# Performance work log

Measured on AMD Instinct MI355X. Metric: run time of the kernel, lower is better.

## Reference

```python
import jax, jax.numpy as jnp
import numpy as np

NUM_ENT = 40000
NUM_REL = 20


def _rgcn_layer(x, src, dst, et, comp, basis, root, bias, act):
    # Basis decomposition: W_r = sum_b comp[r, b] * basis[b]  -> [R, in, out]
    W = jnp.einsum('rb,bio->rio', comp, basis)
    # Per-(dst, relation) sum of source features: equivalent to per-edge
    # transform W_{et[e]} @ x[src[e]] then scatter-sum, but transforms after
    # aggregation (linear, so identical math) to avoid an [E, in, out] gather.
    seg = dst * NUM_REL + et                       # combined segment id
    S = jax.ops.segment_sum(x[src], seg, num_segments=NUM_ENT * NUM_REL)
    S = S.reshape(NUM_ENT, NUM_REL, x.shape[1])    # [N, R, in]
    agg = jnp.einsum('nri,rio->no', S, W)          # [N, out]
    # mean aggregation over ALL incoming edges (PyG RGCNConv aggr='mean')
    deg = jax.ops.segment_sum(jnp.ones(src.shape[0], x.dtype), dst,
                              num_segments=NUM_ENT)
    agg = agg / jnp.clip(deg, 1.0)[:, None]
    out = agg + x @ root + bias
    return jnp.tanh(out) if act else out


def setup_inputs() -> dict:
    key = jax.random.key(0)
    ks = jax.random.split(key, 16)
    E = 640000
    d = 128
    B = 8
    s = 0.05
    return {
        'edge_index': jax.random.randint(ks[0], (2, E), 0, NUM_ENT),
        'edge_type': jax.random.randint(ks[1], (E,), 0, NUM_REL),
        'init_embed': jax.random.normal(ks[2], (NUM_ENT, d), jnp.float32) * s,
        'init_rel': jax.random.normal(ks[3], (NUM_REL * 2, d), jnp.float32) * s,
        'w_rel': jax.random.normal(ks[4], (d, d), jnp.float32) * s,
        'comp1': jax.random.normal(ks[5], (NUM_REL, B), jnp.float32) * s,
        'basis1': jax.random.normal(ks[6], (B, d, d), jnp.float32) * s,
        'root1': jax.random.normal(ks[7], (d, d), jnp.float32) * s,
        'bias1': jax.random.normal(ks[8], (d,), jnp.float32) * s,
        'comp2': jax.random.normal(ks[9], (NUM_REL, B), jnp.float32) * s,
        'basis2': jax.random.normal(ks[10], (B, d, d), jnp.float32) * s,
        'root2': jax.random.normal(ks[11], (d, d), jnp.float32) * s,
        'bias2': jax.random.normal(ks[12], (d,), jnp.float32) * s,
    }


def reference(edge_index, edge_type, init_embed, init_rel, w_rel,
              comp1, basis1, root1, bias1, comp2, basis2, root2, bias2):
    src, dst = edge_index[0], edge_index[1]
    x = init_embed
    # layer 1: init_dim -> gcn_dim, act=tanh (gcn_layer=2)
    x = _rgcn_layer(x, src, dst, edge_type, comp1, basis1, root1, bias1, True)
    # dropout is identity at inference
    # layer 2: embed_dim -> embed_dim, act=None
    x = _rgcn_layer(x, src, dst, edge_type, comp2, basis2, root2, bias2, False)
    r = init_rel @ w_rel
    return (x, r)
```

## Files before the change

kernel.cpp:

```cpp
#include <hip/hip_runtime.h>
#include <hip/hip_bf16.h>

#define NENT 40000
#define NREL 20
#define DIM 128
#define NBASIS 8
#define TILE 16
#define PKCAP 512
#define SCANBLK 157

typedef __attribute__((ext_vector_type(8))) short sh8;
typedef __attribute__((ext_vector_type(4))) float fx4;
typedef __attribute__((ext_vector_type(2))) float f32x2;

__device__ __forceinline__ short f2bf(float f) {
    union { __hip_bfloat16 h; short s; } u;
    u.h = __float2bfloat16(f);
    return u.s;
}

__device__ __forceinline__ void d_tobf(int b, int t, const float* __restrict__ x,
                                       ushort* __restrict__ xb) {
    int i = (b * 256 + t) * 4;
    float4 v = *(const float4*)(x + i);
    ushort4 o;
    o.x = (ushort)f2bf(v.x); o.y = (ushort)f2bf(v.y);
    o.z = (ushort)f2bf(v.z); o.w = (ushort)f2bf(v.w);
    *(ushort4*)(xb + i) = o;
}

__device__ __forceinline__ void d_wfrag9(int b, int tt, const float* __restrict__ basis,
                                         const float* __restrict__ root,
                                         short* __restrict__ Wfb) {
    int t = b * 256 + tt;
    int ks = t / 16384;
    int rem = t & 16383;
    int i = rem >> 7, o = rem & 127;
    float v = (ks < 8) ? basis[ks * 16384 + i * 128 + o] : root[i * 128 + o];
    int c = o >> 4, l15 = o & 15;
    int kk = i >> 5, lhi = (i >> 3) & 3, e = i & 7;
    int lane = l15 + lhi * 16;
    Wfb[(size_t)ks * 16384 + (size_t)(((c * 4 + kk) * 64 + lane) << 3) + e] = f2bf(v);
}

__global__ void k_prep(const float* __restrict__ x, ushort* __restrict__ xb,
                       const float* __restrict__ basis1, const float* __restrict__ root1,
                       short* __restrict__ Wfb1,
                       const float* __restrict__ basis2, const float* __restrict__ root2,
                       short* __restrict__ Wfb2,
                       const int* __restrict__ dst, int E, int* __restrict__ hist,
                       const float* __restrict__ rel, const float* __restrict__ wrel,
                       float* __restrict__ outr, int relrows) {
    int b = blockIdx.x, t = threadIdx.x;
    if (b < 5000) {
        d_tobf(b, t, x, xb);
    } else if (b < 5576) {
        d_wfrag9(b - 5000, t, basis1, root1, Wfb1);
    } else if (b < 6152) {
        d_wfrag9(b - 5576, t, basis2, root2, Wfb2);
    } else if (b < 8652) {
        int e = (b - 6152) * 256 + t;
        if (e < E) atomicAdd(&hist[dst[e]], 1);
    } else {
        int idx = (b - 8652) * 256 + t;
        if (idx < relrows * DIM) {
            int j = idx >> 7, o = idx & 127;
            float s = 0.f;
            for (int i = 0; i < DIM; ++i) s += rel[j * DIM + i] * wrel[i * DIM + o];
            outr[idx] = s;
        }
    }
}

__global__ void k_scan1(const int* __restrict__ hist, int* __restrict__ offs,
                        int* __restrict__ bsum) {
    __shared__ int ps[256];
    int t = threadIdx.x;
    int i = blockIdx.x * 256 + t;
    int v = (i < NENT) ? hist[i] : 0;
    ps[t] = v;
    __syncthreads();
    for (int off = 1; off < 256; off <<= 1) {
        int u = (t >= off) ? ps[t - off] : 0;
        __syncthreads();
        ps[t] += u;
        __syncthreads();
    }
    if (i < NENT) offs[i] = ps[t] - v;
    if (t == 255) bsum[blockIdx.x] = ps[255];
}

__global__ void k_scan2(int* __restrict__ bsum) {
    __shared__ int ps[256];
    int t = threadIdx.x;
    int v = (t < SCANBLK) ? bsum[t] : 0;
    ps[t] = v;
    __syncthreads();
    for (int off = 1; off < 256; off <<= 1) {
        int u = (t >= off) ? ps[t - off] : 0;
        __syncthreads();
        ps[t] += u;
        __syncthreads();
    }
    if (t < SCANBLK) bsum[t] = ps[t] - v;
}

__global__ void k_scan3(int* __restrict__ offs, int* __restrict__ cursor,
                        const int* __restrict__ bsum, int E) {
    int i = blockIdx.x * 256 + threadIdx.x;
    if (i < NENT) {
        int o = offs[i] + bsum[blockIdx.x];
        offs[i] = o;
        cursor[i] = o;
    }
    if (i == 0) offs[NENT] = E;
}

__global__ void k_scatter(const int* __restrict__ et, const int* __restrict__ srcA,
                          const int* __restrict__ dstA, int E,
                          int* __restrict__ cursor, unsigned* __restrict__ packed) {
    int e = blockIdx.x * 256 + threadIdx.x;
    if (e >= E) return;
    int pos = atomicAdd(&cursor[dstA[e]], 1);
    packed[pos] = (unsigned)srcA[e] | ((unsigned)et[e] << 16);
}

#define GLDS(dst, voff, sbase)                                             \
    asm volatile("global_load_dword %0, %1, %2"                            \
                 : "=v"(dst) : "v"(voff), "s"(sbase))

#define WAITV(N)                                                           \
    do {                                                                   \
        asm volatile("s_waitcnt vmcnt(" #N ")" ::: "memory");              \
        __builtin_amdgcn_sched_barrier(0);                                 \
    } while (0)

#define FMA8(AV, CWA, CWB, XP)                                             \
    AV[0] += (f32x2){(CWA).x, (CWA).x} * (XP);                             \
    AV[1] += (f32x2){(CWA).y, (CWA).y} * (XP);                             \
    AV[2] += (f32x2){(CWA).z, (CWA).z} * (XP);                             \
    AV[3] += (f32x2){(CWA).w, (CWA).w} * (XP);                             \
    AV[4] += (f32x2){(CWB).x, (CWB).x} * (XP);                             \
    AV[5] += (f32x2){(CWB).y, (CWB).y} * (XP);                             \
    AV[6] += (f32x2){(CWB).z, (CWB).z} * (XP);                             \
    AV[7] += (f32x2){(CWB).w, (CWB).w} * (XP);

__global__ __launch_bounds__(512) void k_fused(
    const ushort* __restrict__ xb, const unsigned* __restrict__ packed,
    const int* __restrict__ offs, const float* __restrict__ comp,
    const short* __restrict__ Wfb, const float* __restrict__ bias,
    ushort* __restrict__ outbf, float* __restrict__ outf, int act) {
    __shared__ __align__(16) ushort Gl[TILE * 1024];
    __shared__ __align__(16) unsigned pkl[PKCAP];

    int t = threadIdx.x;
    int lane = t & 63, wid = t >> 6;
    unsigned lane4 = (unsigned)(lane * 4);

    int tile0 = blockIdx.x * TILE;
    int base = offs[tile0];
    int totE = offs[tile0 + TILE] - base;
    for (int i = t; i < totE && i < PKCAP; i += 512) pkl[i] = packed[base + i];
    __syncthreads();

    bool fast = (totE <= PKCAP);
    for (int sub = 0; sub < 2; ++sub) {
        int row = wid * 2 + sub;
        int n = tile0 + row;
        int begg = offs[n];
        int cnt = offs[n + 1] - begg;
        int begl = begg - base;

        f32x2 av[NBASIS];
#pragma unroll
        for (int b = 0; b < NBASIS; ++b) av[b] = (f32x2){0.f, 0.f};

        if (cnt > 0 && fast) {
            int sbA[8], seA[8], sbB[8], seB[8];
            unsigned rA[8], rB[8];

            auto ldp = [&](int i0, int (&sb)[8], int (&se)[8]) {
#pragma unroll
                for (int u = 0; u < 8; ++u) {
                    int i = i0 + u;
                    int li = begl + (i < cnt ? i : 0);
                    unsigned p = __builtin_amdgcn_readfirstlane(pkl[li]);
                    sb[u] = (int)(p & 0xFFFFu) * 256;
                    se[u] = (int)(p >> 16);
                }
            };
            auto issue = [&](const int (&sb)[8], unsigned (&r)[8]) {
#pragma unroll
                for (int u = 0; u < 8; ++u) {
                    const char* bp = (const char*)xb + sb[u];
                    GLDS(r[u], lane4, bp);
                }
            };
            auto proc = [&](int i0, const int (&se)[8], const unsigned (&r)[8]) {
#pragma unroll
                for (int u = 0; u < 8; ++u) {
                    if (i0 + u < cnt) {
                        const float4* cp = (const float4*)(comp + se[u] * NBASIS);
                        float4 cwa = cp[0];
                        float4 cwb = cp[1];
                        f32x2 xp = {__uint_as_float(r[u] << 16),
                                    __uint_as_float(r[u] & 0xFFFF0000u)};
                        FMA8(av, cwa, cwb, xp)
                    }
                }
            };

            ldp(0, sbA, seA); issue(sbA, rA);
            int i0 = 0;
            while (i0 < cnt) {
                ldp(i0 + 8, sbB, seB); issue(sbB, rB);
                WAITV(8);
                proc(i0, seA, rA);
                i0 += 8;
                if (i0 >= cnt) break;
                ldp(i0 + 8, sbA, seA); issue(sbA, rA);
                WAITV(8);
                proc(i0, seB, rB);
                i0 += 8;
            }
            asm volatile("s_waitcnt vmcnt(0)" ::: "memory");
            __builtin_amdgcn_sched_barrier(0);
        } else if (cnt > 0) {
            const unsigned* xrow = (const unsigned*)xb + lane;
            unsigned pA = packed[begg], pB = 0, rA = xrow[(size_t)(pA & 0xFFFFu) * 64];
            if (cnt > 1) pB = packed[begg + 1];
            for (int i = 0; i < cnt; ++i) {
                unsigned pC = (i + 2 < cnt) ? packed[begg + i + 2] : 0u;
                unsigned rB = xrow[(size_t)(pB & 0xFFFFu) * 64];
                int et = pA >> 16;
                const float4* cp = (const float4*)(comp + et * NBASIS);
                float4 cwa = cp[0];
                float4 cwb = cp[1];
                f32x2 xp = {__uint_as_float(rA << 16),
                            __uint_as_float(rA & 0xFFFF0000u)};
                FMA8(av, cwa, cwb, xp)
                pA = pB; pB = pC; rA = rB;
            }
        }

        float inv = 1.f / (float)(cnt < 1 ? 1 : cnt);
#pragma unroll
        for (int b = 0; b < NBASIS; ++b) {
            unsigned lo = (unsigned)(ushort)f2bf(av[b][0] * inv);
            unsigned hi = (unsigned)(ushort)f2bf(av[b][1] * inv);
            unsigned byteoff = (unsigned)(row * 2048 + b * 256 + lane * 4);
            byteoff ^= (unsigned)((row & 7) << 4);
            *(unsigned*)((char*)Gl + byteoff) = lo | (hi << 16);
        }
    }
    __syncthreads();

    int l15 = lane & 15, lhi = lane >> 4;
    int c = wid;

    fx4 acc0 = (fx4){0.f, 0.f, 0.f, 0.f};

    const sh8* W8 = (const sh8*)Wfb;

#pragma unroll
    for (int ks = 0; ks < 9; ++ks) {
        sh8 a0f[4];
        if (ks < 8) {
#pragma unroll
            for (int kk = 0; kk < 4; ++kk) {
                int ar0 = l15;
                unsigned bo0 = (unsigned)(ar0 * 2048 + ks * 256 + kk * 64 + lhi * 16);
                bo0 ^= (unsigned)((ar0 & 7) << 4);
                a0f[kk] = *(const sh8*)((const char*)Gl + bo0);
            }
        } else {
#pragma unroll
            for (int kk = 0; kk < 4; ++kk) {
                a0f[kk] = *(const sh8*)(xb + (size_t)(tile0 + l15) * 128 + lhi * 8 + kk * 32);
            }
        }
#pragma unroll
        for (int kk = 0; kk < 4; ++kk) {
            sh8 b = W8[(size_t)ks * 2048 + (size_t)((c * 4 + kk) * 64 + lane)];
            acc0 = __builtin_amdgcn_mfma_f32_16x16x32_bf16(a0f[kk], b, acc0, 0, 0, 0);
        }
    }

    int col = c * 16 + l15;
    float bv = bias[col];
    int orow0 = tile0 + lhi * 4;
#pragma unroll
    for (int j = 0; j < 4; ++j) {
        float v = acc0[j] + bv;
        if (act) {
            v = tanhf(v);
            outbf[(size_t)(orow0 + j) * 128 + col] = (ushort)f2bf(v);
        } else {
            outf[(size_t)(orow0 + j) * 128 + col] = v;
        }
    }
}

extern "C" void kernel_launch(void* const* d_in, const int* in_sizes, int n_in,
                              void* d_out, int out_size, void* d_ws, size_t ws_size,
                              hipStream_t stream) {
    const int* edge_index = (const int*)d_in[0];
    const int* edge_type  = (const int*)d_in[1];
    const float* init_embed = (const float*)d_in[2];
    const float* init_rel   = (const float*)d_in[3];
    const float* w_rel      = (const float*)d_in[4];
    const float* comp1  = (const float*)d_in[5];
    const float* basis1 = (const float*)d_in[6];
    const float* root1  = (const float*)d_in[7];
    const float* bias1  = (const float*)d_in[8];
    const float* comp2  = (const float*)d_in[9];
    const float* basis2 = (const float*)d_in[10];
    const float* root2  = (const float*)d_in[11];
    const float* bias2  = (const float*)d_in[12];

    int E = in_sizes[1];
    const int* src = edge_index;
    const int* dst = edge_index + E;
    int relrows = in_sizes[3] / DIM;

    short* Wfb1 = (short*)d_ws;
    short* Wfb2 = Wfb1 + (size_t)9 * 16384;
    ushort* xb  = (ushort*)(Wfb2 + (size_t)9 * 16384);
    ushort* hb  = xb + (size_t)NENT * DIM;
    int* hist   = (int*)(hb + (size_t)NENT * DIM);
    int* offs   = hist + 40004;
    int* cursor = offs + 40004;
    int* bsum   = cursor + 40004;
    unsigned* packed = (unsigned*)(bsum + 160);

    float* outx = (float*)d_out;
    float* outr = outx + (size_t)NENT * DIM;

    hipMemsetAsync(hist, 0, NENT * sizeof(int), stream);

    int relblocks = (relrows * DIM + 255) / 256;
    k_prep<<<8652 + relblocks, 256, 0, stream>>>(
        init_embed, xb, basis1, root1, Wfb1, basis2, root2, Wfb2,
        dst, E, hist, init_rel, w_rel, outr, relrows);
    k_scan1<<<SCANBLK, 256, 0, stream>>>(hist, offs, bsum);
    k_scan2<<<1, 256, 0, stream>>>(bsum);
    k_scan3<<<SCANBLK, 256, 0, stream>>>(offs, cursor, bsum, E);
    k_scatter<<<(E + 255) / 256, 256, 0, stream>>>(edge_type, src, dst, E, cursor, packed);

    k_fused<<<NENT / TILE, 512, 0, stream>>>(xb, packed, offs, comp1, Wfb1, bias1,
                                             hb, outx, 1);
    k_fused<<<NENT / TILE, 512, 0, stream>>>(hb, packed, offs, comp2, Wfb2, bias2,
                                             hb, outx, 0);
}
```

Measured before the change: 220.9 us.

## Split each destination's edges into two source-half bins and interleave segment processing

The CSR build now bins edges by destination and by which half of the source-node range the source lies in, which doubles the histogram, scan and offset arrays; the block-sum scan is generalized to more than 256 blocks. The fused kernel processes the two rows per wave by interleaving their low-source and high-source segments, so gathers hit a narrower address range at a time. The intent is better cache locality for the source-feature gathers. The cost is a larger scan, extra atomics bins and more bookkeeping.

```diff
diff --git a/kernel.cpp b/kernel.cpp
--- a/kernel.cpp
+++ b/kernel.cpp
@@ -7,7 +7,9 @@
 #define NBASIS 8
 #define TILE 16
 #define PKCAP 512
-#define SCANBLK 157
+#define NBIN (NENT * 2)
+#define SCANBLK 313
+#define SRCHALF (NENT / 2)
 
 typedef __attribute__((ext_vector_type(8))) short sh8;
 typedef __attribute__((ext_vector_type(4))) float fx4;
@@ -48,7 +50,8 @@
                        short* __restrict__ Wfb1,
                        const float* __restrict__ basis2, const float* __restrict__ root2,
                        short* __restrict__ Wfb2,
-                       const int* __restrict__ dst, int E, int* __restrict__ hist,
+                       const int* __restrict__ srcA, const int* __restrict__ dstA,
+                       int E, int* __restrict__ hist,
                        const float* __restrict__ rel, const float* __restrict__ wrel,
                        float* __restrict__ outr, int relrows) {
     int b = blockIdx.x, t = threadIdx.x;
@@ -60,7 +63,10 @@
         d_wfrag9(b - 5576, t, basis2, root2, Wfb2);
     } else if (b < 8652) {
         int e = (b - 6152) * 256 + t;
-        if (e < E) atomicAdd(&hist[dst[e]], 1);
+        if (e < E) {
+            int bin = dstA[e] * 2 + (srcA[e] >= SRCHALF ? 1 : 0);
+            atomicAdd(&hist[bin], 1);
+        }
     } else {
         int idx = (b - 8652) * 256 + t;
         if (idx < relrows * DIM) {
@@ -77,7 +83,7 @@
     __shared__ int ps[256];
     int t = threadIdx.x;
     int i = blockIdx.x * 256 + t;
-    int v = (i < NENT) ? hist[i] : 0;
+    int v = (i < NBIN) ? hist[i] : 0;
     ps[t] = v;
     __syncthreads();
     for (int off = 1; off < 256; off <<= 1) {
@@ -86,15 +92,18 @@
         ps[t] += u;
         __syncthreads();
     }
-    if (i < NENT) offs[i] = ps[t] - v;
+    if (i < NBIN) offs[i] = ps[t] - v;
     if (t == 255) bsum[blockIdx.x] = ps[255];
 }
 
 __global__ void k_scan2(int* __restrict__ bsum) {
     __shared__ int ps[256];
     int t = threadIdx.x;
-    int v = (t < SCANBLK) ? bsum[t] : 0;
-    ps[t] = v;
+    const int chunk = (SCANBLK + 255) / 256;
+    int lo = t * chunk, hi = min(SCANBLK, lo + chunk);
+    int s = 0;
+    for (int i = lo; i < hi; ++i) s += bsum[i];
+    ps[t] = s;
     __syncthreads();
     for (int off = 1; off < 256; off <<= 1) {
         int u = (t >= off) ? ps[t - off] : 0;
@@ -102,18 +111,23 @@
         ps[t] += u;
         __syncthreads();
     }
-    if (t < SCANBLK) bsum[t] = ps[t] - v;
+    int run = (t == 0) ? 0 : ps[t - 1];
+    for (int i = lo; i < hi; ++i) {
+        int v = bsum[i];
+        bsum[i] = run;
+        run += v;
+    }
 }
 
 __global__ void k_scan3(int* __restrict__ offs, int* __restrict__ cursor,
                         const int* __restrict__ bsum, int E) {
     int i = blockIdx.x * 256 + threadIdx.x;
-    if (i < NENT) {
+    if (i < NBIN) {
         int o = offs[i] + bsum[blockIdx.x];
         offs[i] = o;
         cursor[i] = o;
     }
-    if (i == 0) offs[NENT] = E;
+    if (i == 0) offs[NBIN] = E;
 }
 
 __global__ void k_scatter(const int* __restrict__ et, const int* __restrict__ srcA,
@@ -121,7 +135,8 @@
                           int* __restrict__ cursor, unsigned* __restrict__ packed) {
     int e = blockIdx.x * 256 + threadIdx.x;
     if (e >= E) return;
-    int pos = atomicAdd(&cursor[dstA[e]], 1);
+    int bin = dstA[e] * 2 + (srcA[e] >= SRCHALF ? 1 : 0);
+    int pos = atomicAdd(&cursor[bin], 1);
     packed[pos] = (unsigned)srcA[e] | ((unsigned)et[e] << 16);
 }
 
@@ -158,24 +173,27 @@
     unsigned lane4 = (unsigned)(lane * 4);
 
     int tile0 = blockIdx.x * TILE;
-    int base = offs[tile0];
-    int totE = offs[tile0 + TILE] - base;
+    int bin0 = tile0 * 2;
+    int base = offs[bin0];
+    int totE = offs[bin0 + TILE * 2] - base;
     for (int i = t; i < totE && i < PKCAP; i += 512) pkl[i] = packed[base + i];
     __syncthreads();
 
+    int n0b = (tile0 + wid * 2) * 2;
+    int o0 = offs[n0b], o1 = offs[n0b + 1], o2 = offs[n0b + 2],
+        o3 = offs[n0b + 3], o4 = offs[n0b + 4];
+    int cnt0 = o2 - o0, cnt1 = o4 - o2;
+
+    f32x2 av0[NBASIS], av1[NBASIS];
+#pragma unroll
+    for (int b = 0; b < NBASIS; ++b) { av0[b] = (f32x2){0.f, 0.f}; av1[b] = (f32x2){0.f, 0.f}; }
+
     bool fast = (totE <= PKCAP);
-    for (int sub = 0; sub < 2; ++sub) {
-        int row = wid * 2 + sub;
-        int n = tile0 + row;
-        int begg = offs[n];
-        int cnt = offs[n + 1] - begg;
+
+    auto seg = [&](int begg, int cnt, f32x2 (&av)[NBASIS]) {
+        if (cnt <= 0) return;
         int begl = begg - base;
-
-        f32x2 av[NBASIS];
-#pragma unroll
-        for (int b = 0; b < NBASIS; ++b) av[b] = (f32x2){0.f, 0.f};
-
-        if (cnt > 0 && fast) {
+        if (fast) {
             int sbA[8], seA[8], sbB[8], seB[8];
             unsigned rA[8], rB[8];
 
@@ -225,7 +243,7 @@
             }
             asm volatile("s_waitcnt vmcnt(0)" ::: "memory");
             __builtin_amdgcn_sched_barrier(0);
-        } else if (cnt > 0) {
+        } else {
             const unsigned* xrow = (const unsigned*)xb + lane;
             unsigned pA = packed[begg], pB = 0, rA = xrow[(size_t)(pA & 0xFFFFu) * 64];
             if (cnt > 1) pB = packed[begg + 1];
@@ -242,17 +260,30 @@
                 pA = pB; pB = pC; rA = rB;
             }
         }
-
-        float inv = 1.f / (float)(cnt < 1 ? 1 : cnt);
-#pragma unroll
-        for (int b = 0; b < NBASIS; ++b) {
-            unsigned lo = (unsigned)(ushort)f2bf(av[b][0] * inv);
-            unsigned hi = (unsigned)(ushort)f2bf(av[b][1] * inv);
-            unsigned byteoff = (unsigned)(row * 2048 + b * 256 + lane * 4);
-            byteoff ^= (unsigned)((row & 7) << 4);
-            *(unsigned*)((char*)Gl + byteoff) = lo | (hi << 16);
-        }
-    }
+    };
+
+    seg(o0, o1 - o0, av0);
+    seg(o2, o3 - o2, av1);
+    seg(o1, o2 - o1, av0);
+    seg(o3, o4 - o3, av1);
+
+#define WRITEG(AV, SUB, CN)                                                \
+    do {                                                                   \
+        float inv = 1.f / (float)((CN) < 1 ? 1 : (CN));                    \
+        int row = wid * 2 + (SUB);                                         \
+        _Pragma("unroll")                                                  \
+        for (int b = 0; b < NBASIS; ++b) {                                 \
+            unsigned lo = (unsigned)(ushort)f2bf(AV[b][0] * inv);          \
+            unsigned hi = (unsigned)(ushort)f2bf(AV[b][1] * inv);          \
+            unsigned byteoff = (unsigned)(row * 2048 + b * 256 + lane * 4);\
+            byteoff ^= (unsigned)((row & 7) << 4);                         \
+            *(unsigned*)((char*)Gl + byteoff) = lo | (hi << 16);           \
+        }                                                                  \
+    } while (0)
+
+    WRITEG(av0, 0, cnt0);
+    WRITEG(av1, 1, cnt1);
+#undef WRITEG
     __syncthreads();
 
     int l15 = lane & 15, lhi = lane >> 4;
@@ -328,20 +359,20 @@
     ushort* xb  = (ushort*)(Wfb2 + (size_t)9 * 16384);
     ushort* hb  = xb + (size_t)NENT * DIM;
     int* hist   = (int*)(hb + (size_t)NENT * DIM);
-    int* offs   = hist + 40004;
-    int* cursor = offs + 40004;
-    int* bsum   = cursor + 40004;
-    unsigned* packed = (unsigned*)(bsum + 160);
+    int* offs   = hist + 80004;
+    int* cursor = offs + 80004;
+    int* bsum   = cursor + 80004;
+    unsigned* packed = (unsigned*)(bsum + 320);
 
     float* outx = (float*)d_out;
     float* outr = outx + (size_t)NENT * DIM;
 
-    hipMemsetAsync(hist, 0, NENT * sizeof(int), stream);
+    hipMemsetAsync(hist, 0, NBIN * sizeof(int), stream);
 
     int relblocks = (relrows * DIM + 255) / 256;
     k_prep<<<8652 + relblocks, 256, 0, stream>>>(
         init_embed, xb, basis1, root1, Wfb1, basis2, root2, Wfb2,
-        dst, E, hist, init_rel, w_rel, outr, relrows);
+        src, dst, E, hist, init_rel, w_rel, outr, relrows);
     k_scan1<<<SCANBLK, 256, 0, stream>>>(hist, offs, bsum);
     k_scan2<<<1, 256, 0, stream>>>(bsum);
     k_scan3<<<SCANBLK, 256, 0, stream>>>(offs, cursor, bsum, E);
```

Result: slower. 246.9 us (+11.8%).
